# Kernel optimization log

Measured on AMD Instinct MI355X. Metric: run time of the kernel, lower is better.

## Reference

```python
import math
import jax, jax.numpy as jnp
import numpy as np

NUM_HEADS = 16
TAU_RCS, LAMBDA_RCS = 2.0, 0.6
PATCH = 16
PREFIX = 8
GAUSS_STD = 5.0


def gaussian_window(d1, d2, std):
    c = 1.0 / (std * math.sqrt(2.0))
    k1 = (jnp.arange(d1, dtype=jnp.float32) - (d1 - 1) / 2.0) * c
    k2 = (jnp.arange(d2, dtype=jnp.float32) - (d2 - 1) / 2.0) * c
    return jnp.exp(-(k1[:, None] ** 2 + k2[None, :] ** 2))  # [d1, d2]


def attention_addition(d1, d2, prefix, std):
    # out[(a,b),(c,d)] = window[a-c+d1-1, b-d+d2-1]  (conv of delta images with window)
    win = gaussian_window(2 * d1 - 1, 2 * d2 - 1, std)
    ia = jnp.arange(d1)
    jb = jnp.arange(d2)
    r = ia[:, None] - ia[None, :] + (d1 - 1)   # [d1, d1]
    s = jb[:, None] - jb[None, :] + (d2 - 1)   # [d2, d2]
    add = win[r[:, None, :, None], s[None, :, None, :]]  # [d1,d2,d1,d2]
    add = add.reshape(d1 * d2, d1 * d2)
    add = jnp.pad(add, ((prefix, 0), (prefix, 0)))  # zero rows/cols for prefix tokens
    return add[None]  # [1, N, N]


def setup_inputs() -> dict:
    key = jax.random.key(0)
    ks = jax.random.split(key, 5)
    B, C = 4, 1024
    d1 = d2 = 512 // PATCH  # 32
    N = d1 * d2 + PREFIX    # 1032
    H = NUM_HEADS
    x = jax.random.normal(ks[0], (B, N, C), dtype=jnp.float32)
    qkv_w = jax.random.normal(ks[1], (3 * C, C), dtype=jnp.float32) * 0.02
    qkv_b = jnp.zeros((3 * C,), dtype=jnp.float32)
    proj_w = jax.random.normal(ks[2], (C, C), dtype=jnp.float32) * 0.02
    proj_b = jnp.zeros((C,), dtype=jnp.float32)
    attn_add = attention_addition(d1, d2, PREFIX, GAUSS_STD)
    # stored RCS attention maps are softmax outputs -> row-normalized positives
    rcs = jax.random.uniform(ks[3], (B * H, N, N), dtype=jnp.float32)
    rcs = rcs / jnp.sum(rcs, axis=-1, keepdims=True)
    return {"x": x, "qkv_w": qkv_w, "qkv_b": qkv_b, "proj_w": proj_w,
            "proj_b": proj_b, "attn_addition": attn_add, "rcs_attn": rcs}


def reference(x, qkv_w, qkv_b, proj_w, proj_b, attn_addition, rcs_attn):
    B, N, C = x.shape
    H = NUM_HEADS
    hd = C // H
    scale = hd ** -0.5
    qkv = jnp.einsum('bnc,dc->bnd', x, qkv_w) + qkv_b  # [B,N,3C]
    q, k, v = jnp.split(qkv, 3, axis=-1)
    def to_heads(t):
        return t.reshape(B, N, H, hd).transpose(0, 2, 1, 3).reshape(B * H, N, hd)
    k = to_heads(k)
    v = to_heads(v)
    # custom K-K attention with additive Gaussian bias
    attn = jnp.einsum('bnd,bmd->bnm', k, k) * scale + attn_addition
    attn = jax.nn.softmax(attn, axis=-1)
    # RCS blending with stored intermediate attention maps
    attn = TAU_RCS * ((1.0 - LAMBDA_RCS) * attn + LAMBDA_RCS * rcs_attn)
    out = jnp.einsum('bnm,bmd->bnd', attn, v)  # [B*H, N, hd]
    out = out.reshape(B, H, N, hd).transpose(0, 2, 1, 3).reshape(B, N, C)
    out = jnp.einsum('bnc,dc->bnd', out, proj_w) + proj_b
    return out
```

## Files before the change

### kernel.cpp

```cpp
#include <hip/hip_runtime.h>
#include <stdint.h>

#define NSEQ 1032
#define CDIM 1024
#define HD 64
#define H_HEADS 16
#define BROWS 4128
#define SCALE 0.125f

typedef __attribute__((ext_vector_type(8))) short bf16x8;
typedef __attribute__((ext_vector_type(4))) float f32x4;

__device__ __forceinline__ unsigned short f2bf(float f) {
  union { float f; uint32_t u; } c; c.f = f;
  uint32_t u = c.u;
  return (unsigned short)((u + 0x7fffu + ((u >> 16) & 1u)) >> 16);
}

__device__ __forceinline__ void gl16(const void* gp, void* lp) {
  __builtin_amdgcn_global_load_lds((const __attribute__((address_space(1))) void*)gp,
                                   (__attribute__((address_space(3))) void*)lp, 16, 0, 0);
}

__global__ void convert_f32_bf16(const float* __restrict__ src, unsigned short* __restrict__ dst, int n4) {
  int i = blockIdx.x * blockDim.x + threadIdx.x;
  if (i >= n4) return;
  float4 v = ((const float4*)src)[i];
  ushort4 o;
  o.x = f2bf(v.x); o.y = f2bf(v.y); o.z = f2bf(v.z); o.w = f2bf(v.w);
  ((ushort4*)dst)[i] = o;
}

template<int MODE>
__global__ __launch_bounds__(256, 2) void gemm_bt(
    const unsigned short* __restrict__ A,
    const unsigned short* __restrict__ Bw,
    const float* __restrict__ bias,
    unsigned short* __restrict__ outK,
    unsigned short* __restrict__ outV,
    float* __restrict__ outF,
    int M, int K)
{
  __shared__ unsigned short As[128 * 32];
  __shared__ unsigned short Bs[128 * 32];
  const int t = threadIdx.x;
  const int w = t >> 6, lane = t & 63, lr = lane & 15, lg = lane >> 4;
  const int wr = w >> 1, wc = w & 1;
  const int m0 = blockIdx.y * 128, n0 = blockIdx.x * 128;
  f32x4 acc[4][4] = {};

  for (int ks = 0; ks < K; ks += 32) {
    #pragma unroll
    for (int q = 0; q < 2; ++q) {
      const int o = t + (q << 8);
      const int row = o >> 2, kc = o & 3;
      int ra = m0 + row; ra = ra < M ? ra : M - 1;
      gl16(A + (size_t)ra * K + ks + kc * 8, (void*)(As + o * 8));
      gl16(Bw + (size_t)(n0 + row) * K + ks + kc * 8, (void*)(Bs + o * 8));
    }
    __syncthreads();
    bf16x8 af[4], bfr[4];
    #pragma unroll
    for (int m = 0; m < 4; ++m)
      af[m] = *(const bf16x8*)(As + (wr * 64 + m * 16 + lr) * 32 + lg * 8);
    #pragma unroll
    for (int n = 0; n < 4; ++n)
      bfr[n] = *(const bf16x8*)(Bs + (wc * 64 + n * 16 + lr) * 32 + lg * 8);
    #pragma unroll
    for (int m = 0; m < 4; ++m)
      #pragma unroll
      for (int n = 0; n < 4; ++n)
        acc[m][n] = __builtin_amdgcn_mfma_f32_16x16x32_bf16(af[m], bfr[n], acc[m][n], 0, 0, 0);
    __syncthreads();
  }

  #pragma unroll
  for (int m = 0; m < 4; ++m) {
    const int rowb = m0 + wr * 64 + m * 16 + lg * 4;
    #pragma unroll
    for (int n = 0; n < 4; ++n) {
      const int col = n0 + wc * 64 + n * 16 + lr;
      const float bv = bias[col];
      #pragma unroll
      for (int r = 0; r < 4; ++r) {
        const int row = rowb + r;
        if (row >= M) continue;
        const float v = acc[m][n][r] + bv;
        if (MODE == 0) {
          const int b = row / NSEQ, nn = row - b * NSEQ;
          if (col < CDIM) {
            const int h = col >> 6, d = col & 63;
            outK[((size_t)(b * H_HEADS + h) * NSEQ + nn) * HD + d] = f2bf(v);
          } else {
            const int jj = col - CDIM, h = jj >> 6, d = jj & 63;
            outV[((size_t)(b * H_HEADS + h) * HD + d) * NSEQ + nn] = f2bf(v);
          }
        } else {
          outF[(size_t)row * CDIM + col] = v;
        }
      }
    }
  }
}

__global__ __launch_bounds__(256, 3) void attn_fused(
    const unsigned short* __restrict__ Kb,
    const unsigned short* __restrict__ Vt,
    const float* __restrict__ rcs,
    unsigned short* __restrict__ outp)
{
  __shared__ __align__(16) unsigned short Kc[2][64 * 64];
  __shared__ __align__(16) unsigned short Vs[2][64 * 64];
  __shared__ __align__(16) unsigned short As[64 * 72];
  __shared__ unsigned short Ps[64 * 72];
  const int t = threadIdx.x;
  const int w = t >> 6, lane = t & 63, lr = lane & 15, lg = lane >> 4;
  const int bid = blockIdx.x;
  const int nb = (bid & 7) * 136 + (bid >> 3);
  const int bh = nb / 17, rt = nb - bh * 17;
  const int i_base = rt * 64 + w * 16;
  const int arow = w * 16 + lr;
  const float* rbase = rcs + (size_t)bh * NSEQ * NSEQ;
  const unsigned short* kbase = Kb + (size_t)bh * NSEQ * HD;
  const unsigned short* vbase = Vt + (size_t)bh * HD * NSEQ;

  const unsigned short* srck[2]; int dok[2];
  const unsigned short* srcv[2]; int dov[2];
  #pragma unroll
  for (int q = 0; q < 2; ++q) {
    const int p = t + (q << 8);
    const int row = p >> 3, sch = p & 7;
    const int gch = (sch ^ row) & 7;
    srck[q] = kbase + (size_t)row * HD + gch * 8;  dok[q] = p * 8;
    srcv[q] = vbase + (size_t)row * NSEQ + gch * 8; dov[q] = p * 8;
  }
  auto stage_kv = [&](int tB, int buf) {
    #pragma unroll
    for (int q = 0; q < 2; ++q) gl16(srck[q] + (size_t)tB * HD, (void*)(Kc[buf] + dok[q]));
    #pragma unroll
    for (int q = 0; q < 2; ++q) gl16(srcv[q] + tB, (void*)(Vs[buf] + dov[q]));
  };
  auto stage_kv_tail = [&](int buf) {
    const int tB = 1024;
    #pragma unroll
    for (int q = 0; q < 2; ++q) {
      const int p = t + (q << 8);
      const int row = p >> 3, sch = p & 7;
      const int gch = (sch ^ row) & 7;
      int mrow = tB + row; if (mrow > NSEQ - 1) mrow = NSEQ - 1;
      gl16(kbase + (size_t)mrow * HD + gch * 8, (void*)(Kc[buf] + p * 8));
    }
    #pragma unroll
    for (int q = 0; q < 2; ++q) {
      const int p = t + (q << 8);
      const int row = p >> 3, sch = p & 7;
      const int gch = (sch ^ row) & 7;
      int gc = tB + gch * 8; if (gc > NSEQ - 8) gc = NSEQ - 8;
      gl16(vbase + (size_t)row * NSEQ + gc, (void*)(Vs[buf] + p * 8));
    }
  };

  const int ccol = (lane & 15) * 4;
  const float* rsrc[4]; int lrow_loc[4];
  #pragma unroll
  for (int j = 0; j < 4; ++j) {
    lrow_loc[j] = w * 16 + j * 4 + (lane >> 4);
    int grow = rt * 64 + lrow_loc[j]; if (grow > NSEQ - 1) grow = NSEQ - 1;
    rsrc[j] = rbase + (size_t)grow * NSEQ;
  }
  f32x4 rreg[4];
  auto ld_rcs = [&](int tB) {
    int gcol = tB + ccol; if (gcol > NSEQ - 4) gcol = NSEQ - 4;
    #pragma unroll
    for (int j = 0; j < 4; ++j) rreg[j] = *(const f32x4*)(rsrc[j] + gcol);
  };
  auto wr_rcs = [&]() {
    #pragma unroll
    for (int j = 0; j < 4; ++j) {
      ushort4 o;
      o.x = f2bf(rreg[j][0]); o.y = f2bf(rreg[j][1]);
      o.z = f2bf(rreg[j][2]); o.w = f2bf(rreg[j][3]);
      *(ushort4*)(As + lrow_loc[j] * 72 + ccol) = o;
    }
  };

  bf16x8 akr[2];
  {
    int row = i_base + lr; if (row > NSEQ - 1) row = NSEQ - 1;
    const unsigned short* p = kbase + (size_t)row * HD + lg * 8;
    akr[0] = *(const bf16x8*)(p);
    akr[1] = *(const bf16x8*)(p + 32);
  }

  const int irow_base = i_base + lg * 4;
  float u[16], v[16];
  {
    #pragma unroll
    for (int fn = 0; fn < 4; ++fn) {
      const int x = 16 * fn + lr;
      const int m1_0 = ((x + 24) >> 5) - 1;
      const int m2 = (x - 8) & 31;
      #pragma unroll
      for (int r = 0; r < 4; ++r) {
        const int irow = irow_base + r;
        const int ip = irow - 8;
        const int i1 = ip >> 5, j1 = ip & 31;
        const int di = i1 - m1_0, dj = j1 - m2;
        const float iok = (irow >= 8) ? 1.f : 0.f;
        u[fn * 4 + r] = __expf(-0.02f * (float)(di * di + dj * dj)) * iok;
        v[fn * 4 + r] = __expf(0.08f * (float)di);
      }
    }
  }
  const float C1 = 0.92311634639f;
  const float C2 = 0.85214378896f;

  f32x4 accP[4] = {};
  f32x4 accR[4] = {};
  float lsum[4] = {0.f, 0.f, 0.f, 0.f};

  ld_rcs(0);
  stage_kv(0, 0);
  wr_rcs();
  asm volatile("s_waitcnt vmcnt(0)");
  __builtin_amdgcn_s_barrier();
  __builtin_amdgcn_sched_barrier(0);

  for (int mt = 0; mt < 17; ++mt) {
    const int mB = mt * 64;
    const int cur = mt & 1, nxt = cur ^ 1;

    if (mt < 16)       ld_rcs(mB + 64);
    if (mt < 15)       stage_kv(mB + 64, nxt);
    else if (mt == 15) stage_kv_tail(nxt);

    const unsigned short* kc = Kc[cur];
    const unsigned short* vsb = Vs[cur];

    __builtin_amdgcn_s_setprio(1);
    f32x4 s[4];
    #pragma unroll
    for (int fn = 0; fn < 4; ++fn) {
      const int row = 16 * fn + lr;
      const int r7 = row & 7;
      f32x4 z = {0.f, 0.f, 0.f, 0.f};
      bf16x8 b0 = *(const bf16x8*)(kc + row * 64 + ((lg ^ r7) & 7) * 8);
      bf16x8 b1 = *(const bf16x8*)(kc + row * 64 + (((4 + lg) ^ r7) & 7) * 8);
      z = __builtin_amdgcn_mfma_f32_16x16x32_bf16(akr[0], b0, z, 0, 0, 0);
      z = __builtin_amdgcn_mfma_f32_16x16x32_bf16(akr[1], b1, z, 0, 0, 0);
      s[fn] = z;
    }
    __builtin_amdgcn_s_setprio(0);

    #pragma unroll
    for (int fn = 0; fn < 4; ++fn) {
      const int mcol = mB + 16 * fn + lr;
      const float mok = (mcol >= 8 && mcol < NSEQ) ? 1.f : 0.f;
      const bool mlt = (mcol < NSEQ);
      #pragma unroll
      for (int r = 0; r < 4; ++r) {
        const int fi = fn * 4 + r;
        const float sv = s[fn][r] * SCALE + u[fi] * mok;
        const float p = mlt ? __expf(sv) : 0.f;
        lsum[r] += p;
        Ps[(w * 16 + lg * 4 + r) * 72 + 16 * fn + lr] = f2bf(p);
        u[fi] *= v[fi] * C1;
        v[fi] *= C2;
      }
    }

    bf16x8 af[2];
    #pragma unroll
    for (int kf = 0; kf < 2; ++kf) {
      const int kg = mB + kf * 32 + lg * 8;
      if (kg + 8 <= NSEQ) {
        af[kf] = *(const bf16x8*)(As + arow * 72 + kf * 32 + lg * 8);
      } else {
        #pragma unroll
        for (int j = 0; j < 8; ++j) af[kf][j] = 0;
      }
    }

    bf16x8 pa0 = *(const bf16x8*)(Ps + (w * 16 + lr) * 72 + lg * 8);
    bf16x8 pa1 = *(const bf16x8*)(Ps + (w * 16 + lr) * 72 + 32 + lg * 8);
    __builtin_amdgcn_s_setprio(1);
    #pragma unroll
    for (int fd = 0; fd < 4; ++fd) {
      const int row = 16 * fd + lr;
      const int r7 = row & 7;
      bf16x8 v0 = *(const bf16x8*)(vsb + row * 64 + ((lg ^ r7) & 7) * 8);
      bf16x8 v1 = *(const bf16x8*)(vsb + row * 64 + (((4 + lg) ^ r7) & 7) * 8);
      accP[fd] = __builtin_amdgcn_mfma_f32_16x16x32_bf16(pa0, v0, accP[fd], 0, 0, 0);
      accP[fd] = __builtin_amdgcn_mfma_f32_16x16x32_bf16(pa1, v1, accP[fd], 0, 0, 0);
      accR[fd] = __builtin_amdgcn_mfma_f32_16x16x32_bf16(af[0], v0, accR[fd], 0, 0, 0);
      accR[fd] = __builtin_amdgcn_mfma_f32_16x16x32_bf16(af[1], v1, accR[fd], 0, 0, 0);
    }
    __builtin_amdgcn_s_setprio(0);

    if (mt < 16) wr_rcs();

    __builtin_amdgcn_sched_barrier(0);
    asm volatile("s_waitcnt vmcnt(0)");
    __builtin_amdgcn_s_barrier();
    __builtin_amdgcn_sched_barrier(0);
  }

  #pragma unroll
  for (int r = 0; r < 4; ++r) {
    float vv = lsum[r];
    vv += __shfl_xor(vv, 1); vv += __shfl_xor(vv, 2);
    vv += __shfl_xor(vv, 4); vv += __shfl_xor(vv, 8);
    lsum[r] = vv;
  }

  const int b = bh >> 4, hh = bh & 15;
  #pragma unroll
  for (int fd = 0; fd < 4; ++fd) {
    #pragma unroll
    for (int r = 0; r < 4; ++r) {
      const int irow = i_base + lg * 4 + r;
      if (irow < NSEQ) {
        const float val = 0.8f * accP[fd][r] / lsum[r] + 1.2f * accR[fd][r];
        outp[(size_t)(b * NSEQ + irow) * CDIM + hh * 64 + 16 * fd + lr] = f2bf(val);
      }
    }
  }
}

extern "C" void kernel_launch(void* const* d_in, const int* in_sizes, int n_in,
                              void* d_out, int out_size, void* d_ws, size_t ws_size,
                              hipStream_t stream) {
  (void)in_sizes; (void)n_in; (void)out_size; (void)ws_size;
  const float* x      = (const float*)d_in[0];
  const float* qkv_w  = (const float*)d_in[1];
  const float* qkv_b  = (const float*)d_in[2];
  const float* proj_w = (const float*)d_in[3];
  const float* proj_b = (const float*)d_in[4];
  const float* rcs    = (const float*)d_in[6];
  float* out = (float*)d_out;

  char* ws = (char*)d_ws;
  unsigned short* x_bf = (unsigned short*)ws; ws += (size_t)BROWS * CDIM * 2;
  unsigned short* wkv  = (unsigned short*)ws; ws += (size_t)2048 * CDIM * 2;
  unsigned short* wp   = (unsigned short*)ws; ws += (size_t)1024 * CDIM * 2;
  unsigned short* Kb   = (unsigned short*)ws; ws += (size_t)64 * NSEQ * HD * 2;
  unsigned short* Vt   = (unsigned short*)ws; ws += (size_t)64 * HD * NSEQ * 2;
  unsigned short* op   = (unsigned short*)ws; ws += (size_t)BROWS * CDIM * 2;

  const int n1 = BROWS * CDIM / 4, n2 = 2048 * CDIM / 4, n3 = 1024 * CDIM / 4;
  convert_f32_bf16<<<(n1 + 255) / 256, 256, 0, stream>>>(x, x_bf, n1);
  convert_f32_bf16<<<(n2 + 255) / 256, 256, 0, stream>>>(qkv_w + 1024 * 1024, wkv, n2);
  convert_f32_bf16<<<(n3 + 255) / 256, 256, 0, stream>>>(proj_w, wp, n3);

  gemm_bt<0><<<dim3(16, 33), 256, 0, stream>>>(x_bf, wkv, qkv_b + 1024, Kb, Vt, nullptr, BROWS, CDIM);
  attn_fused<<<1088, 256, 0, stream>>>(Kb, Vt, rcs, op);
  gemm_bt<1><<<dim3(8, 33), 256, 0, stream>>>(op, wp, proj_b, nullptr, nullptr, out, BROWS, CDIM);
}
```

Before: 178.1 us.

## Load RCS directly into MFMA A-fragments, transpose S tile, per-wave P buffers

The RCS tile no longer goes through a shared As buffer. Each lane now loads the RCS elements matching its MFMA A-operand layout straight into registers and converts them in place, and the prefetch is issued after the softmax so its latency is hidden behind compute with a partial vmcnt wait. The QK MFMA operands are swapped so each lane owns one query row, which makes lsum a per-lane scalar and lets the Gaussian bias be computed by a running formula instead of per-element u/v recurrences. P now sits in per-wave swizzled shared buffers, cutting shared memory enough to raise launch bounds to 4 blocks per CU. This trades extra exp calls and tighter register pressure against the removed LDS round trip.

```diff
diff --git a/kernel.cpp b/kernel.cpp
--- a/kernel.cpp
+++ b/kernel.cpp
@@ -103,7 +103,7 @@
   }
 }
 
-__global__ __launch_bounds__(256, 3) void attn_fused(
+__global__ __launch_bounds__(256, 4) void attn_fused(
     const unsigned short* __restrict__ Kb,
     const unsigned short* __restrict__ Vt,
     const float* __restrict__ rcs,
@@ -111,18 +111,17 @@
 {
   __shared__ __align__(16) unsigned short Kc[2][64 * 64];
   __shared__ __align__(16) unsigned short Vs[2][64 * 64];
-  __shared__ __align__(16) unsigned short As[64 * 72];
-  __shared__ unsigned short Ps[64 * 72];
+  __shared__ __align__(16) unsigned short Ps[4][16 * 64];
   const int t = threadIdx.x;
   const int w = t >> 6, lane = t & 63, lr = lane & 15, lg = lane >> 4;
   const int bid = blockIdx.x;
   const int nb = (bid & 7) * 136 + (bid >> 3);
   const int bh = nb / 17, rt = nb - bh * 17;
   const int i_base = rt * 64 + w * 16;
-  const int arow = w * 16 + lr;
   const float* rbase = rcs + (size_t)bh * NSEQ * NSEQ;
   const unsigned short* kbase = Kb + (size_t)bh * NSEQ * HD;
   const unsigned short* vbase = Vt + (size_t)bh * HD * NSEQ;
+  unsigned short* psw = &Ps[w][0];
 
   const unsigned short* srck[2]; int dok[2];
   const unsigned short* srcv[2]; int dov[2];
@@ -160,68 +159,49 @@
     }
   };
 
-  const int ccol = (lane & 15) * 4;
-  const float* rsrc[4]; int lrow_loc[4];
-  #pragma unroll
-  for (int j = 0; j < 4; ++j) {
-    lrow_loc[j] = w * 16 + j * 4 + (lane >> 4);
-    int grow = rt * 64 + lrow_loc[j]; if (grow > NSEQ - 1) grow = NSEQ - 1;
-    rsrc[j] = rbase + (size_t)grow * NSEQ;
-  }
+  int irow_c = i_base + lr; if (irow_c > NSEQ - 1) irow_c = NSEQ - 1;
+  const float* rrow = rbase + (size_t)irow_c * NSEQ;
+  const int cba = 8 * lg;
   f32x4 rreg[4];
   auto ld_rcs = [&](int tB) {
-    int gcol = tB + ccol; if (gcol > NSEQ - 4) gcol = NSEQ - 4;
-    #pragma unroll
-    for (int j = 0; j < 4; ++j) rreg[j] = *(const f32x4*)(rsrc[j] + gcol);
-  };
-  auto wr_rcs = [&]() {
-    #pragma unroll
-    for (int j = 0; j < 4; ++j) {
-      ushort4 o;
-      o.x = f2bf(rreg[j][0]); o.y = f2bf(rreg[j][1]);
-      o.z = f2bf(rreg[j][2]); o.w = f2bf(rreg[j][3]);
-      *(ushort4*)(As + lrow_loc[j] * 72 + ccol) = o;
+    #pragma unroll
+    for (int q = 0; q < 4; ++q) {
+      int col = tB + (q >> 1) * 32 + cba + (q & 1) * 4;
+      if (col > NSEQ - 4) col = NSEQ - 4;
+      rreg[q] = *(const f32x4*)(rrow + col);
     }
   };
 
   bf16x8 akr[2];
   {
-    int row = i_base + lr; if (row > NSEQ - 1) row = NSEQ - 1;
-    const unsigned short* p = kbase + (size_t)row * HD + lg * 8;
+    const unsigned short* p = kbase + (size_t)irow_c * HD + lg * 8;
     akr[0] = *(const bf16x8*)(p);
     akr[1] = *(const bf16x8*)(p + 32);
   }
 
-  const int irow_base = i_base + lg * 4;
-  float u[16], v[16];
-  {
-    #pragma unroll
-    for (int fn = 0; fn < 4; ++fn) {
-      const int x = 16 * fn + lr;
-      const int m1_0 = ((x + 24) >> 5) - 1;
+  const int ii = i_base + lr;
+  const int ip = ii - 8;
+  const int j1 = ip & 31;
+  float a_run = (float)(ip >> 5);
+  const float e_lg = (lg < 2) ? 1.f : 0.f;
+  const float ibad = (ii >= 8) ? 0.f : -1e30f;
+  float cdj[16];
+  #pragma unroll
+  for (int fn = 0; fn < 4; ++fn)
+    #pragma unroll
+    for (int r = 0; r < 4; ++r) {
+      const int x = 16 * fn + 4 * lg + r;
       const int m2 = (x - 8) & 31;
-      #pragma unroll
-      for (int r = 0; r < 4; ++r) {
-        const int irow = irow_base + r;
-        const int ip = irow - 8;
-        const int i1 = ip >> 5, j1 = ip & 31;
-        const int di = i1 - m1_0, dj = j1 - m2;
-        const float iok = (irow >= 8) ? 1.f : 0.f;
-        u[fn * 4 + r] = __expf(-0.02f * (float)(di * di + dj * dj)) * iok;
-        v[fn * 4 + r] = __expf(0.08f * (float)di);
-      }
-    }
-  }
-  const float C1 = 0.92311634639f;
-  const float C2 = 0.85214378896f;
+      const float dj = (float)(j1 - m2);
+      cdj[fn * 4 + r] = -0.02f * dj * dj + ibad;
+    }
 
   f32x4 accP[4] = {};
   f32x4 accR[4] = {};
-  float lsum[4] = {0.f, 0.f, 0.f, 0.f};
-
+  float lsum = 0.f;
+
+  stage_kv(0, 0);
   ld_rcs(0);
-  stage_kv(0, 0);
-  wr_rcs();
   asm volatile("s_waitcnt vmcnt(0)");
   __builtin_amdgcn_s_barrier();
   __builtin_amdgcn_sched_barrier(0);
@@ -230,15 +210,14 @@
     const int mB = mt * 64;
     const int cur = mt & 1, nxt = cur ^ 1;
 
-    if (mt < 16)       ld_rcs(mB + 64);
     if (mt < 15)       stage_kv(mB + 64, nxt);
     else if (mt == 15) stage_kv_tail(nxt);
+    __builtin_amdgcn_sched_barrier(0);
 
     const unsigned short* kc = Kc[cur];
     const unsigned short* vsb = Vs[cur];
-
     __builtin_amdgcn_s_setprio(1);
-    f32x4 s[4];
+    f32x4 st[4];
     #pragma unroll
     for (int fn = 0; fn < 4; ++fn) {
       const int row = 16 * fn + lr;
@@ -246,43 +225,73 @@
       f32x4 z = {0.f, 0.f, 0.f, 0.f};
       bf16x8 b0 = *(const bf16x8*)(kc + row * 64 + ((lg ^ r7) & 7) * 8);
       bf16x8 b1 = *(const bf16x8*)(kc + row * 64 + (((4 + lg) ^ r7) & 7) * 8);
-      z = __builtin_amdgcn_mfma_f32_16x16x32_bf16(akr[0], b0, z, 0, 0, 0);
-      z = __builtin_amdgcn_mfma_f32_16x16x32_bf16(akr[1], b1, z, 0, 0, 0);
-      s[fn] = z;
+      z = __builtin_amdgcn_mfma_f32_16x16x32_bf16(b0, akr[0], z, 0, 0, 0);
+      z = __builtin_amdgcn_mfma_f32_16x16x32_bf16(b1, akr[1], z, 0, 0, 0);
+      st[fn] = z;
     }
     __builtin_amdgcn_s_setprio(0);
 
-    #pragma unroll
-    for (int fn = 0; fn < 4; ++fn) {
-      const int mcol = mB + 16 * fn + lr;
-      const float mok = (mcol >= 8 && mcol < NSEQ) ? 1.f : 0.f;
-      const bool mlt = (mcol < NSEQ);
+    {
+      const float d0 = a_run + e_lg;
+      const float d1 = a_run;
+      const float d2 = d0 - 1.f;
+      const float d3 = d1 - 1.f;
+      const float qd[4] = { -0.02f * d0 * d0, -0.02f * d1 * d1,
+                            -0.02f * d2 * d2, -0.02f * d3 * d3 };
       #pragma unroll
-      for (int r = 0; r < 4; ++r) {
-        const int fi = fn * 4 + r;
-        const float sv = s[fn][r] * SCALE + u[fi] * mok;
-        const float p = mlt ? __expf(sv) : 0.f;
-        lsum[r] += p;
-        Ps[(w * 16 + lg * 4 + r) * 72 + 16 * fn + lr] = f2bf(p);
-        u[fi] *= v[fi] * C1;
-        v[fi] *= C2;
-      }
+      for (int fn = 0; fn < 4; ++fn) {
+        float pv[4];
+        #pragma unroll
+        for (int r = 0; r < 4; ++r) {
+          float ad = __expf(qd[fn] + cdj[fn * 4 + r]);
+          if (mt == 0 && fn == 0) ad = (lg < 2) ? 0.f : ad;
+          float p = __expf(st[fn][r] * SCALE + ad);
+          if (mt == 16) {
+            if (fn > 0) p = 0.f; else p = (lg < 2) ? p : 0.f;
+          }
+          lsum += p;
+          pv[r] = p;
+        }
+        const int chunk = (2 * fn + (lg >> 1)) ^ (lr & 7);
+        const int off = 4 * (lg & 1);
+        uint32_t w0 = (uint32_t)f2bf(pv[0]) | ((uint32_t)f2bf(pv[1]) << 16);
+        uint32_t w1 = (uint32_t)f2bf(pv[2]) | ((uint32_t)f2bf(pv[3]) << 16);
+        *(uint32_t*)(psw + lr * 64 + chunk * 8 + off)     = w0;
+        *(uint32_t*)(psw + lr * 64 + chunk * 8 + off + 2) = w1;
+      }
+      a_run -= 2.f;
     }
 
     bf16x8 af[2];
-    #pragma unroll
-    for (int kf = 0; kf < 2; ++kf) {
-      const int kg = mB + kf * 32 + lg * 8;
-      if (kg + 8 <= NSEQ) {
-        af[kf] = *(const bf16x8*)(As + arow * 72 + kf * 32 + lg * 8);
-      } else {
+    {
+      if (mt == 16) {
         #pragma unroll
-        for (int j = 0; j < 8; ++j) af[kf][j] = 0;
-      }
-    }
-
-    bf16x8 pa0 = *(const bf16x8*)(Ps + (w * 16 + lr) * 72 + lg * 8);
-    bf16x8 pa1 = *(const bf16x8*)(Ps + (w * 16 + lr) * 72 + 32 + lg * 8);
+        for (int q = 0; q < 4; ++q) {
+          const bool valid = (q < 2) && (lg == 0);
+          if (!valid) {
+            #pragma unroll
+            for (int j = 0; j < 4; ++j) rreg[q][j] = 0.f;
+          }
+        }
+      }
+      #pragma unroll
+      for (int kf = 0; kf < 2; ++kf) {
+        f32x4 lo = rreg[2 * kf], hi = rreg[2 * kf + 1];
+        bf16x8 a;
+        a[0] = (short)f2bf(lo[0]); a[1] = (short)f2bf(lo[1]);
+        a[2] = (short)f2bf(lo[2]); a[3] = (short)f2bf(lo[3]);
+        a[4] = (short)f2bf(hi[0]); a[5] = (short)f2bf(hi[1]);
+        a[6] = (short)f2bf(hi[2]); a[7] = (short)f2bf(hi[3]);
+        af[kf] = a;
+      }
+    }
+    __builtin_amdgcn_sched_barrier(0);
+
+    if (mt < 16) ld_rcs(mB + 64);
+    __builtin_amdgcn_sched_barrier(0);
+
+    bf16x8 pa0 = *(const bf16x8*)(psw + lr * 64 + ((lg ^ (lr & 7)) & 7) * 8);
+    bf16x8 pa1 = *(const bf16x8*)(psw + lr * 64 + (((4 + lg) ^ (lr & 7)) & 7) * 8);
     __builtin_amdgcn_s_setprio(1);
     #pragma unroll
     for (int fd = 0; fd < 4; ++fd) {
@@ -297,21 +306,17 @@
     }
     __builtin_amdgcn_s_setprio(0);
 
-    if (mt < 16) wr_rcs();
-
-    __builtin_amdgcn_sched_barrier(0);
-    asm volatile("s_waitcnt vmcnt(0)");
+    __builtin_amdgcn_sched_barrier(0);
+    asm volatile("s_waitcnt vmcnt(4)");
     __builtin_amdgcn_s_barrier();
     __builtin_amdgcn_sched_barrier(0);
   }
 
-  #pragma unroll
-  for (int r = 0; r < 4; ++r) {
-    float vv = lsum[r];
-    vv += __shfl_xor(vv, 1); vv += __shfl_xor(vv, 2);
-    vv += __shfl_xor(vv, 4); vv += __shfl_xor(vv, 8);
-    lsum[r] = vv;
-  }
+  lsum += __shfl_xor(lsum, 16);
+  lsum += __shfl_xor(lsum, 32);
+  float ls[4];
+  #pragma unroll
+  for (int r = 0; r < 4; ++r) ls[r] = __shfl(lsum, 4 * lg + r);
 
   const int b = bh >> 4, hh = bh & 15;
   #pragma unroll
@@ -320,7 +325,7 @@
     for (int r = 0; r < 4; ++r) {
       const int irow = i_base + lg * 4 + r;
       if (irow < NSEQ) {
-        const float val = 0.8f * accP[fd][r] / lsum[r] + 1.2f * accR[fd][r];
+        const float val = 0.8f * accP[fd][r] / ls[r] + 1.2f * accR[fd][r];
         outp[(size_t)(b * NSEQ + irow) * CDIM + hh * 64 + 16 * fd + lr] = f2bf(val);
       }
     }
```

Result: slower. 226.1 us (+27.0%).

## Prefetch RCS tiles two iterations ahead with double register buffers

Applied to the files above, without the earlier changes.

The RCS global loads now run two tiles ahead in two alternating register sets, and the main loop is unrolled by two so each set has a fixed name. Each iteration waits with vmcnt(4) instead of vmcnt(0), so the next RCS load can stay in flight across the barrier while the KV stage must finish. This hides more of the fp32 RCS stream latency behind the MFMA work, at the cost of extra VGPRs under the 3-blocks-per-SM launch bound and more fragile wait-count bookkeeping.

```diff
diff --git a/kernel.cpp b/kernel.cpp
--- a/kernel.cpp
+++ b/kernel.cpp
@@ -103,6 +103,22 @@
   }
 }
 
+#define LD_RCS(tB, rr) do {                                            \
+    int col0 = (tB) + ccol; if (col0 > NSEQ - 4) col0 = NSEQ - 4;      \
+    _Pragma("unroll")                                                  \
+    for (int j = 0; j < 4; ++j) rr[j] = *(const f32x4*)(rsrc[j] + col0); \
+  } while (0)
+
+#define WR_RCS(rr) do {                                                \
+    _Pragma("unroll")                                                  \
+    for (int j = 0; j < 4; ++j) {                                      \
+      ushort4 o;                                                       \
+      o.x = f2bf(rr[j][0]); o.y = f2bf(rr[j][1]);                      \
+      o.z = f2bf(rr[j][2]); o.w = f2bf(rr[j][3]);                      \
+      *(ushort4*)(Asm + lrow_loc[j] * 72 + ccol) = o;                  \
+    }                                                                  \
+  } while (0)
+
 __global__ __launch_bounds__(256, 3) void attn_fused(
     const unsigned short* __restrict__ Kb,
     const unsigned short* __restrict__ Vt,
@@ -111,7 +127,7 @@
 {
   __shared__ __align__(16) unsigned short Kc[2][64 * 64];
   __shared__ __align__(16) unsigned short Vs[2][64 * 64];
-  __shared__ __align__(16) unsigned short As[64 * 72];
+  __shared__ __align__(16) unsigned short Asm[64 * 72];
   __shared__ unsigned short Ps[64 * 72];
   const int t = threadIdx.x;
   const int w = t >> 6, lane = t & 63, lr = lane & 15, lg = lane >> 4;
@@ -168,21 +184,7 @@
     int grow = rt * 64 + lrow_loc[j]; if (grow > NSEQ - 1) grow = NSEQ - 1;
     rsrc[j] = rbase + (size_t)grow * NSEQ;
   }
-  f32x4 rreg[4];
-  auto ld_rcs = [&](int tB) {
-    int gcol = tB + ccol; if (gcol > NSEQ - 4) gcol = NSEQ - 4;
-    #pragma unroll
-    for (int j = 0; j < 4; ++j) rreg[j] = *(const f32x4*)(rsrc[j] + gcol);
-  };
-  auto wr_rcs = [&]() {
-    #pragma unroll
-    for (int j = 0; j < 4; ++j) {
-      ushort4 o;
-      o.x = f2bf(rreg[j][0]); o.y = f2bf(rreg[j][1]);
-      o.z = f2bf(rreg[j][2]); o.w = f2bf(rreg[j][3]);
-      *(ushort4*)(As + lrow_loc[j] * 72 + ccol) = o;
-    }
-  };
+  f32x4 rregA[4], rregB[4];
 
   bf16x8 akr[2];
   {
@@ -194,22 +196,20 @@
 
   const int irow_base = i_base + lg * 4;
   float u[16], v[16];
-  {
-    #pragma unroll
-    for (int fn = 0; fn < 4; ++fn) {
-      const int x = 16 * fn + lr;
-      const int m1_0 = ((x + 24) >> 5) - 1;
-      const int m2 = (x - 8) & 31;
-      #pragma unroll
-      for (int r = 0; r < 4; ++r) {
-        const int irow = irow_base + r;
-        const int ip = irow - 8;
-        const int i1 = ip >> 5, j1 = ip & 31;
-        const int di = i1 - m1_0, dj = j1 - m2;
-        const float iok = (irow >= 8) ? 1.f : 0.f;
-        u[fn * 4 + r] = __expf(-0.02f * (float)(di * di + dj * dj)) * iok;
-        v[fn * 4 + r] = __expf(0.08f * (float)di);
-      }
+  #pragma unroll
+  for (int fn = 0; fn < 4; ++fn) {
+    const int x = 16 * fn + lr;
+    const int m1_0 = ((x + 24) >> 5) - 1;
+    const int m2 = (x - 8) & 31;
+    #pragma unroll
+    for (int r = 0; r < 4; ++r) {
+      const int irow = irow_base + r;
+      const int ip = irow - 8;
+      const int i1 = ip >> 5, j1 = ip & 31;
+      const int di = i1 - m1_0, dj = j1 - m2;
+      const float iok = (irow >= 8) ? 1.f : 0.f;
+      u[fn * 4 + r] = __expf(-0.02f * (float)(di * di + dj * dj)) * iok;
+      v[fn * 4 + r] = __expf(0.08f * (float)di);
     }
   }
   const float C1 = 0.92311634639f;
@@ -219,21 +219,9 @@
   f32x4 accR[4] = {};
   float lsum[4] = {0.f, 0.f, 0.f, 0.f};
 
-  ld_rcs(0);
-  stage_kv(0, 0);
-  wr_rcs();
-  asm volatile("s_waitcnt vmcnt(0)");
-  __builtin_amdgcn_s_barrier();
-  __builtin_amdgcn_sched_barrier(0);
-
-  for (int mt = 0; mt < 17; ++mt) {
+  auto compute_tile = [&](int mt) {
     const int mB = mt * 64;
-    const int cur = mt & 1, nxt = cur ^ 1;
-
-    if (mt < 16)       ld_rcs(mB + 64);
-    if (mt < 15)       stage_kv(mB + 64, nxt);
-    else if (mt == 15) stage_kv_tail(nxt);
-
+    const int cur = mt & 1;
     const unsigned short* kc = Kc[cur];
     const unsigned short* vsb = Vs[cur];
 
@@ -274,7 +262,7 @@
     for (int kf = 0; kf < 2; ++kf) {
       const int kg = mB + kf * 32 + lg * 8;
       if (kg + 8 <= NSEQ) {
-        af[kf] = *(const bf16x8*)(As + arow * 72 + kf * 32 + lg * 8);
+        af[kf] = *(const bf16x8*)(Asm + arow * 72 + kf * 32 + lg * 8);
       } else {
         #pragma unroll
         for (int j = 0; j < 8; ++j) af[kf][j] = 0;
@@ -296,13 +284,43 @@
       accR[fd] = __builtin_amdgcn_mfma_f32_16x16x32_bf16(af[1], v1, accR[fd], 0, 0, 0);
     }
     __builtin_amdgcn_s_setprio(0);
-
-    if (mt < 16) wr_rcs();
-
-    __builtin_amdgcn_sched_barrier(0);
-    asm volatile("s_waitcnt vmcnt(0)");
-    __builtin_amdgcn_s_barrier();
-    __builtin_amdgcn_sched_barrier(0);
+  };
+
+  stage_kv(0, 0);
+  LD_RCS(0, rregA);
+  LD_RCS(64, rregB);
+  WR_RCS(rregA);
+  asm volatile("s_waitcnt vmcnt(4)");
+  __builtin_amdgcn_s_barrier();
+  __builtin_amdgcn_sched_barrier(0);
+
+  for (int it = 0; it < 9; ++it) {
+    {
+      const int mt = 2 * it, mB = mt * 64;
+      if (mt < 15)       stage_kv(mB + 64, 1);
+      else if (mt == 15) stage_kv_tail(1);
+      if (mt < 15)       LD_RCS(mB + 128, rregA);
+      compute_tile(mt);
+      if (mt < 16)       WR_RCS(rregB);
+      __builtin_amdgcn_sched_barrier(0);
+      if (mt < 15)       { asm volatile("s_waitcnt vmcnt(4)"); }
+      else if (mt == 15) { asm volatile("s_waitcnt vmcnt(0)"); }
+      if (mt < 16) { __builtin_amdgcn_s_barrier(); __builtin_amdgcn_sched_barrier(0); }
+    }
+    if (it == 8) break;
+    {
+      const int mt = 2 * it + 1, mB = mt * 64;
+      if (mt < 15)       stage_kv(mB + 64, 0);
+      else if (mt == 15) stage_kv_tail(0);
+      if (mt < 15)       LD_RCS(mB + 128, rregB);
+      compute_tile(mt);
+      WR_RCS(rregA);
+      __builtin_amdgcn_sched_barrier(0);
+      if (mt < 15)       { asm volatile("s_waitcnt vmcnt(4)"); }
+      else               { asm volatile("s_waitcnt vmcnt(0)"); }
+      __builtin_amdgcn_s_barrier();
+      __builtin_amdgcn_sched_barrier(0);
+    }
   }
 
   #pragma unroll
```

New measurement: 391.9 us. 2.2x slower.
